# Kernel optimization log

Measured on AMD Instinct MI355X. Metric: run time of the kernel, lower is better.

Reference implementation:

```python
import jax, jax.numpy as jnp
import numpy as np

B, C, H, W = 32, 64, 56, 56
REPN, NK, SMALL = 50, 17, 3   # repN=64-int(64*0.23), nk=ceil(51/3)
GROUPS = 4                     # N_rep
EPS = 1e-5


def _build_index_mats():
    """Reduce the fallback's python scatter-add loops to exact linear maps.
    For flat position p=r*NK+j the roll shifts depend only on p%3, so each
    shift class s gets a (REPN,NK) count matrix over source nk-slots."""
    rng = np.random.RandomState(123)
    ghost = np.sort(rng.choice(C, C - REPN, replace=False))
    rep = np.array(sorted(set(range(C)) - set(ghost.tolist())), np.int32)
    Mh = np.zeros((3, REPN, NK), np.int32)
    Mv = np.zeros((3, REPN, NK), np.int32)
    Mid = np.zeros((REPN, NK), np.int32)
    for _ in range(GROUPS):
        for r in range(REPN):
            perm = rng.permutation(NK)
            for p in range(NK):
                Mh[(r * NK + p) % 3, r, perm[p]] += 1
        for r in range(REPN):
            perm = rng.permutation(NK)
            for p in range(NK):
                Mv[(r * NK + p) % 3, r, perm[p]] += 1
        kk = rng.randint(0, NK, REPN)
        for r in range(REPN):
            Mid[r, kk[r]] += 1
    return ghost.astype(np.int32), rep, Mh, Mv, Mid


def setup_inputs() -> dict:
    key = jax.random.key(0)
    k1, k2, k3 = jax.random.split(key, 3)
    ghost, rep, Mh, Mv, Mid = _build_index_mats()
    return {
        "inputs": jax.random.normal(k1, (B, C, H, W), jnp.float32),
        "w0": jax.random.normal(k2, (REPN * NK, 1, SMALL, SMALL), jnp.float32) * 0.1,
        "w1": jax.random.normal(k3, (REPN * NK, 1, SMALL, SMALL), jnp.float32) * 0.1,
        "Mh": jnp.asarray(Mh), "Mv": jnp.asarray(Mv), "Mid": jnp.asarray(Mid),
        "ghost_idx": jnp.asarray(ghost), "rep_idx": jnp.asarray(rep),
    }


def _bn(x):
    # BatchNorm2d in training mode, affine weight=1 / bias=0 (init values)
    m = x.mean(axis=(0, 2, 3), keepdims=True)
    v = x.var(axis=(0, 2, 3), keepdims=True)
    return (x - m) / jnp.sqrt(v + EPS)


def reference(inputs, w0, w1, Mh, Mv, Mid, ghost_idx, rep_idx):
    rep_in = inputs[:, rep_idx]      # (B, REPN, H, W)
    ghost_in = inputs[:, ghost_idx]  # (B, ghostN, H, W)

    def conv(w):  # depthwise-grouped conv: groups=REPN, each 1->NK channels
        return jax.lax.conv_general_dilated(
            rep_in, w, window_strides=(1, 1), padding=((2, 2), (2, 2)),
            dimension_numbers=('NCHW', 'OIHW', 'NCHW'),
            feature_group_count=REPN)

    out = conv(w0) + conv(w1)                       # (B, REPN*NK, H+2, W+2)
    xv = out.reshape(B, REPN, NK, H + 2, W + 2)

    Mhf, Mvf, Midf = (m.astype(xv.dtype) for m in (Mh, Mv, Mid))
    sh1, sw1 = (0, 1, 2), (0, 2, 1)   # lora1: shifts (i%3, 2i%3)
    sh2, sw2 = (0, 2, 1), (0, 1, 2)   # lora2: shifts (2i%3, i%3)

    lora1 = sum(jnp.roll(jnp.einsum('rk,brkhw->brhw', Mhf[s], xv),
                         (sh1[s], sw1[s]), axis=(2, 3)) for s in range(3))
    lora2 = sum(jnp.roll(jnp.einsum('rk,brkhw->brhw', Mvf[s], xv),
                         (sh2[s], sw2[s]), axis=(2, 3)) for s in range(3))
    small = jnp.einsum('rk,brkhw->brhw', Midf, xv)

    # center-crop back to (H, W): dh = dw = 1
    lora1 = lora1[:, :, 1:1 + H, 1:1 + W]
    lora2 = lora2[:, :, 1:1 + H, 1:1 + W]
    small = small[:, :, 1:1 + H, 1:1 + W]

    x = _bn(lora1) + _bn(lora2) + _bn(small) + rep_in
    return jnp.concatenate([x, ghost_in], axis=1)   # (B, C, H, W)
```

## Files before the change

### kernel.cpp

```cpp
#include <hip/hip_runtime.h>

#define Bn 32
#define Cn 64
#define Hn 56
#define Wn 56
#define REPN 50
#define NKn 17
#define HWn (Hn*Wn)
#define NSTATf 100352.0f
#define EPSf 1e-5f

#define PART_OFF 0
#define WEFF_OFF 9600

#define SEGH 7
#define NTASK 112

__global__ void k_weff(const float* __restrict__ w0, const float* __restrict__ w1,
                       const int* __restrict__ Mh, const int* __restrict__ Mv,
                       const int* __restrict__ Mid, float* __restrict__ ws)
{
    int idx = blockIdx.x * blockDim.x + threadIdx.x;
    if (idx >= REPN*63) return;
    int r   = idx / 63;
    int rem = idx % 63;
    int t   = rem / 9;
    int ij  = rem % 9;
    const int* M = (t < 3) ? (Mh + (t*REPN + r)*NKn)
                 : (t < 6) ? (Mv + ((t-3)*REPN + r)*NKn)
                           : (Mid + r*NKn);
    float acc = 0.f;
    #pragma unroll
    for (int k = 0; k < NKn; ++k)
        acc += (float)M[k] * (w0[(r*NKn + k)*9 + ij] + w1[(r*NKn + k)*9 + ij]);
    ws[WEFF_OFF + idx] = acc;
}

__device__ __forceinline__ void load_row8c(const float* __restrict__ ch, int row, int q,
                                           float* __restrict__ X, float& c55)
{
    bool rv = (row >= 0) && (row < Hn);
    int rc = rv ? row : 0;
    const float* rp = ch + rc*Wn;
    float4 c0 = *(const float4*)(rp + (q ? 4*q - 4 : 0));
    float4 c1 = *(const float4*)(rp + 4*q);
    int ox = (4*q + 4 <= 55) ? 4*q + 4 : 55;
    float cx = rp[ox];
    float mr = rv ? 1.f : 0.f;
    float m0 = (rv && q > 0)  ? 1.f : 0.f;
    float mx = (rv && q < 13) ? 1.f : 0.f;
    X[0]=c0.y*m0; X[1]=c0.z*m0; X[2]=c0.w*m0;
    X[3]=c1.x*mr; X[4]=c1.y*mr; X[5]=c1.z*mr; X[6]=c1.w*mr;
    X[7]=cx*mx;
    c55 = (q == 0) ? rp[55]*mr : 0.f;
}

template <typename F>
__device__ __forceinline__ void conv_walk(const float* __restrict__ ch,
        const float (&wk)[63], int tid, F emit)
{
    if (tid >= NTASK) return;
    int seg = tid / 14;
    int q   = tid - seg*14;
    int h0  = seg * SEGH;
    bool top = (seg == 0);

    float W[5][8], C[5], T[8];
    {
        float dummy;
        if (top) load_row8c(ch, 55, q, T, dummy);
    }
    #pragma unroll
    for (int k = 0; k < 5; ++k)
        load_row8c(ch, h0 - 3 + k, q, W[k], C[k]);

    #pragma unroll
    for (int s = 0; s < SEGH; ++s) {
        int h = h0 + s;
        float Wn8[8], Cn1;
        load_row8c(ch, h + 2, q, Wn8, Cn1);

        float l1[4], l2[4], sm[4];
        #pragma unroll
        for (int p = 0; p < 4; ++p) { l1[p]=0.f; l2[p]=0.f; sm[p]=0.f; }
        #pragma unroll
        for (int i = 0; i < 3; ++i)
            #pragma unroll
            for (int j = 0; j < 3; ++j) {
                float wh0 = wk[i*3+j],    wv0 = wk[27+i*3+j], wid = wk[54+i*3+j];
                float wh1 = wk[9+i*3+j],  wv2 = wk[45+i*3+j];
                float wh2 = wk[18+i*3+j], wv1 = wk[36+i*3+j];
                #pragma unroll
                for (int p = 0; p < 4; ++p) {
                    float a  = W[2+i][p+2+j];
                    l1[p] = fmaf(a, wh0, l1[p]);
                    l2[p] = fmaf(a, wv0, l2[p]);
                    sm[p] = fmaf(a, wid, sm[p]);
                    float bA = W[1+i][p+j];
                    l1[p] = fmaf(bA, wh1, l1[p]);
                    l2[p] = fmaf(bA, wv2, l2[p]);
                    float bB = W[i][p+1+j];
                    l1[p] = fmaf(bB, wh2, l1[p]);
                    l2[p] = fmaf(bB, wv1, l2[p]);
                }
            }
        if (q == 0) {
            #pragma unroll
            for (int i = 0; i < 3; ++i) {
                l1[0] = fmaf(C[1+i], wk[9+3*i],  l1[0]);
                l2[0] = fmaf(C[1+i], wk[45+3*i], l2[0]);
            }
        }
        if (s == 0 && top) {
            #pragma unroll
            for (int j = 0; j < 3; ++j)
                #pragma unroll
                for (int p = 0; p < 4; ++p) {
                    l1[p] = fmaf(T[p+1+j], wk[18+j], l1[p]);
                    l2[p] = fmaf(T[p+1+j], wk[36+j], l2[p]);
                }
        }
        float res[4] = {W[3][3], W[3][4], W[3][5], W[3][6]};
        emit(h, q, l1, l2, sm, res);

        #pragma unroll
        for (int k = 0; k < 4; ++k) {
            #pragma unroll
            for (int x = 0; x < 8; ++x) W[k][x] = W[k+1][x];
            C[k] = C[k+1];
        }
        #pragma unroll
        for (int x = 0; x < 8; ++x) W[4][x] = Wn8[x];
        C[4] = Cn1;
    }
}

__global__ void __launch_bounds__(128) k_stats(const float* __restrict__ in,
        const int* __restrict__ rep_idx, float* __restrict__ ws)
{
    int bid = blockIdx.x;
    int r = bid % REPN;
    int b = bid / REPN;
    int tid = threadIdx.x;

    const float* wr = ws + WEFF_OFF + r*63;
    float wk[63];
    #pragma unroll
    for (int i = 0; i < 63; ++i) wk[i] = wr[i];

    int cin = rep_idx[r];
    const float* ch = in + ((size_t)(b*Cn + cin))*HWn;

    float s1=0.f,q1=0.f,s2=0.f,q2=0.f,s3=0.f,q3=0.f;
    conv_walk(ch, wk, tid,
        [&](int h, int q, float* l1, float* l2, float* sm, float* res) {
            (void)h; (void)q; (void)res;
            #pragma unroll
            for (int p = 0; p < 4; ++p) {
                s1 += l1[p]; q1 += l1[p]*l1[p];
                s2 += l2[p]; q2 += l2[p]*l2[p];
                s3 += sm[p]; q3 += sm[p]*sm[p];
            }
        });

    __shared__ float red[2][6];
    float vals[6] = {s1,q1,s2,q2,s3,q3};
    int lane = tid & 63, wave = tid >> 6;
    #pragma unroll
    for (int v = 0; v < 6; ++v) {
        float x = vals[v];
        for (int o = 32; o; o >>= 1) x += __shfl_down(x, o, 64);
        if (lane == 0) red[wave][v] = x;
    }
    __syncthreads();
    if (tid < 6)
        ws[PART_OFF + (tid*REPN + r)*Bn + b] = red[0][tid] + red[1][tid];
}

__global__ void __launch_bounds__(128) k_out(const float* __restrict__ in,
        const int* __restrict__ rep_idx, const int* __restrict__ ghost_idx,
        const float* __restrict__ ws, float* __restrict__ out)
{
    int bid = blockIdx.x;
    int c = bid % Cn;
    int b = bid / Cn;
    int tid = threadIdx.x;

    if (c >= REPN) {
        int cin = ghost_idx[c - REPN];
        const float4* s4 = (const float4*)(in + ((size_t)(b*Cn + cin))*HWn);
        float4* d4 = (float4*)(out + ((size_t)(b*Cn + c))*HWn);
        for (int i = tid; i < HWn/4; i += 128) d4[i] = s4[i];
        return;
    }

    int r = c;
    __shared__ float sred[6];
    if (tid < 6) {
        const float* pp = ws + PART_OFF + (tid*REPN + r)*Bn;
        float s = 0.f;
        #pragma unroll
        for (int i = 0; i < Bn; ++i) s += pp[i];
        sred[tid] = s;
    }
    __syncthreads();
    const float inv = 1.0f / NSTATf;
    float m1 = sred[0]*inv, v1 = sred[1]*inv - m1*m1;
    float m2 = sred[2]*inv, v2 = sred[3]*inv - m2*m2;
    float m3 = sred[4]*inv, v3 = sred[5]*inv - m3*m3;
    float r1 = rsqrtf(v1 + EPSf), r2 = rsqrtf(v2 + EPSf), r3 = rsqrtf(v3 + EPSf);

    const float* wr = ws + WEFF_OFF + r*63;
    float wk[63];
    #pragma unroll
    for (int i = 0; i < 63; ++i) wk[i] = wr[i];

    int cin = rep_idx[r];
    const float* ch = in + ((size_t)(b*Cn + cin))*HWn;
    float* dst = out + ((size_t)(b*Cn + c))*HWn;

    conv_walk(ch, wk, tid,
        [&](int h, int q, float* l1, float* l2, float* sm, float* res) {
            float4 o;
            o.x = (l1[0]-m1)*r1 + (l2[0]-m2)*r2 + (sm[0]-m3)*r3 + res[0];
            o.y = (l1[1]-m1)*r1 + (l2[1]-m2)*r2 + (sm[1]-m3)*r3 + res[1];
            o.z = (l1[2]-m1)*r1 + (l2[2]-m2)*r2 + (sm[2]-m3)*r3 + res[2];
            o.w = (l1[3]-m1)*r1 + (l2[3]-m2)*r2 + (sm[3]-m3)*r3 + res[3];
            *(float4*)(dst + h*Wn + 4*q) = o;
        });
}

extern "C" void kernel_launch(void* const* d_in, const int* in_sizes, int n_in,
                              void* d_out, int out_size, void* d_ws, size_t ws_size,
                              hipStream_t stream) {
    const float* in   = (const float*)d_in[0];
    const float* w0   = (const float*)d_in[1];
    const float* w1   = (const float*)d_in[2];
    const int*   Mh   = (const int*)d_in[3];
    const int*   Mv   = (const int*)d_in[4];
    const int*   Mid  = (const int*)d_in[5];
    const int*   ghost= (const int*)d_in[6];
    const int*   rep  = (const int*)d_in[7];
    float* out  = (float*)d_out;
    float* ws   = (float*)d_ws;

    k_weff<<<(REPN*63 + 127)/128, 128, 0, stream>>>(w0, w1, Mh, Mv, Mid, ws);
    k_stats<<<Bn*REPN, 128, 0, stream>>>(in, rep, ws);
    k_out<<<Bn*Cn, 128, 0, stream>>>(in, rep, ghost, ws, out);
}
```

Measured before the change: 124.7 us.

## Fuse weight, stats and output kernels into one cooperative persistent kernel

Replaces the three-kernel launch chain with a single cooperative kernel of 1024 blocks that uses grid-wide syncs between the effective-weight, batch-stat and output phases. Each block handles two (batch, channel) slices and falls back to the old launches if occupancy is below four blocks per CU or the cooperative launch fails. The goal is to remove launch gaps and inter-kernel idle time. In exchange, the fixed grid of 1024 blocks with 112 active threads each may limit parallelism, and grid.sync adds its own overhead.

New measurement: 124.3 us. Within noise of the previous version (-0.3%).

```diff
diff --git a/kernel.cpp b/kernel.cpp
--- a/kernel.cpp
+++ b/kernel.cpp
@@ -1,4 +1,7 @@
 #include <hip/hip_runtime.h>
+#include <hip/hip_cooperative_groups.h>
+
+namespace cg = cooperative_groups;
 
 #define Bn 32
 #define Cn 64
@@ -16,12 +19,11 @@
 #define SEGH 7
 #define NTASK 112
 
-__global__ void k_weff(const float* __restrict__ w0, const float* __restrict__ w1,
-                       const int* __restrict__ Mh, const int* __restrict__ Mv,
-                       const int* __restrict__ Mid, float* __restrict__ ws)
-{
-    int idx = blockIdx.x * blockDim.x + threadIdx.x;
-    if (idx >= REPN*63) return;
+__device__ __forceinline__ void weff_one(int idx,
+        const float* __restrict__ w0, const float* __restrict__ w1,
+        const int* __restrict__ Mh, const int* __restrict__ Mv,
+        const int* __restrict__ Mid, float* __restrict__ ws)
+{
     int r   = idx / 63;
     int rem = idx % 63;
     int t   = rem / 9;
@@ -34,6 +36,14 @@
     for (int k = 0; k < NKn; ++k)
         acc += (float)M[k] * (w0[(r*NKn + k)*9 + ij] + w1[(r*NKn + k)*9 + ij]);
     ws[WEFF_OFF + idx] = acc;
+}
+
+__global__ void k_weff(const float* __restrict__ w0, const float* __restrict__ w1,
+                       const int* __restrict__ Mh, const int* __restrict__ Mv,
+                       const int* __restrict__ Mid, float* __restrict__ ws)
+{
+    int idx = blockIdx.x * blockDim.x + threadIdx.x;
+    if (idx < REPN*63) weff_one(idx, w0, w1, Mh, Mv, Mid, ws);
 }
 
 __device__ __forceinline__ void load_row8c(const float* __restrict__ ch, int row, int q,
@@ -135,6 +145,112 @@
     }
 }
 
+__global__ void __launch_bounds__(128, 2) k_fused(const float* __restrict__ in,
+        const float* __restrict__ w0, const float* __restrict__ w1,
+        const int* __restrict__ Mh, const int* __restrict__ Mv,
+        const int* __restrict__ Mid,
+        const int* __restrict__ rep_idx, const int* __restrict__ ghost_idx,
+        float* __restrict__ ws, float* __restrict__ out)
+{
+    cg::grid_group grid = cg::this_grid();
+    int tid = threadIdx.x;
+
+    {
+        int gidx = blockIdx.x * 128 + tid;
+        if (gidx < REPN*63) weff_one(gidx, w0, w1, Mh, Mv, Mid, ws);
+    }
+    grid.sync();
+
+    __shared__ float red[2][6];
+    #pragma unroll
+    for (int it = 0; it < 2; ++it) {
+        int v = blockIdx.x*2 + it;
+        int c = v & 63;
+        int b = v >> 6;
+        if (c >= REPN) {
+            int cin = ghost_idx[c - REPN];
+            const float4* s4 = (const float4*)(in + ((size_t)(b*Cn + cin))*HWn);
+            float4* d4 = (float4*)(out + ((size_t)(b*Cn + c))*HWn);
+            for (int i = tid; i < HWn/4; i += 128) d4[i] = s4[i];
+            continue;
+        }
+        int r = c;
+        const float* wr = ws + WEFF_OFF + r*63;
+        float wk[63];
+        #pragma unroll
+        for (int i = 0; i < 63; ++i) wk[i] = wr[i];
+        const float* ch = in + ((size_t)(b*Cn + rep_idx[r]))*HWn;
+
+        float s1=0.f,q1=0.f,s2=0.f,q2=0.f,s3=0.f,q3=0.f;
+        conv_walk(ch, wk, tid,
+            [&](int h, int q, float* l1, float* l2, float* sm, float* res) {
+                (void)h; (void)q; (void)res;
+                #pragma unroll
+                for (int p = 0; p < 4; ++p) {
+                    s1 += l1[p]; q1 += l1[p]*l1[p];
+                    s2 += l2[p]; q2 += l2[p]*l2[p];
+                    s3 += sm[p]; q3 += sm[p]*sm[p];
+                }
+            });
+        __syncthreads();
+        {
+            float vals[6] = {s1,q1,s2,q2,s3,q3};
+            int lane = tid & 63, wave = tid >> 6;
+            #pragma unroll
+            for (int x = 0; x < 6; ++x) {
+                float y = vals[x];
+                for (int o = 32; o; o >>= 1) y += __shfl_down(y, o, 64);
+                if (lane == 0) red[wave][x] = y;
+            }
+        }
+        __syncthreads();
+        if (tid < 6)
+            ws[PART_OFF + (tid*REPN + r)*Bn + b] = red[0][tid] + red[1][tid];
+    }
+    grid.sync();
+
+    __shared__ float sred[6];
+    #pragma unroll
+    for (int it = 0; it < 2; ++it) {
+        int v = blockIdx.x*2 + it;
+        int c = v & 63;
+        int b = v >> 6;
+        if (c >= REPN) continue;
+        int r = c;
+        __syncthreads();
+        if (tid < 6) {
+            const float* pp = ws + PART_OFF + (tid*REPN + r)*Bn;
+            float s = 0.f;
+            #pragma unroll
+            for (int i = 0; i < Bn; ++i) s += pp[i];
+            sred[tid] = s;
+        }
+        __syncthreads();
+        const float inv = 1.0f / NSTATf;
+        float m1 = sred[0]*inv, v1 = sred[1]*inv - m1*m1;
+        float m2 = sred[2]*inv, v2 = sred[3]*inv - m2*m2;
+        float m3 = sred[4]*inv, v3 = sred[5]*inv - m3*m3;
+        float r1 = rsqrtf(v1 + EPSf), r2 = rsqrtf(v2 + EPSf), r3 = rsqrtf(v3 + EPSf);
+
+        const float* wr = ws + WEFF_OFF + r*63;
+        float wk[63];
+        #pragma unroll
+        for (int i = 0; i < 63; ++i) wk[i] = wr[i];
+        const float* ch = in + ((size_t)(b*Cn + rep_idx[r]))*HWn;
+        float* dst = out + ((size_t)(b*Cn + c))*HWn;
+
+        conv_walk(ch, wk, tid,
+            [&](int h, int q, float* l1, float* l2, float* sm, float* res) {
+                float4 o;
+                o.x = (l1[0]-m1)*r1 + (l2[0]-m2)*r2 + (sm[0]-m3)*r3 + res[0];
+                o.y = (l1[1]-m1)*r1 + (l2[1]-m2)*r2 + (sm[1]-m3)*r3 + res[1];
+                o.z = (l1[2]-m1)*r1 + (l2[2]-m2)*r2 + (sm[2]-m3)*r3 + res[2];
+                o.w = (l1[3]-m1)*r1 + (l2[3]-m2)*r2 + (sm[3]-m3)*r3 + res[3];
+                *(float4*)(dst + h*Wn + 4*q) = o;
+            });
+    }
+}
+
 __global__ void __launch_bounds__(128) k_stats(const float* __restrict__ in,
         const int* __restrict__ rep_idx, float* __restrict__ ws)
 {
@@ -147,9 +263,7 @@
     float wk[63];
     #pragma unroll
     for (int i = 0; i < 63; ++i) wk[i] = wr[i];
-
-    int cin = rep_idx[r];
-    const float* ch = in + ((size_t)(b*Cn + cin))*HWn;
+    const float* ch = in + ((size_t)(b*Cn + rep_idx[r]))*HWn;
 
     float s1=0.f,q1=0.f,s2=0.f,q2=0.f,s3=0.f,q3=0.f;
     conv_walk(ch, wk, tid,
@@ -214,9 +328,7 @@
     float wk[63];
     #pragma unroll
     for (int i = 0; i < 63; ++i) wk[i] = wr[i];
-
-    int cin = rep_idx[r];
-    const float* ch = in + ((size_t)(b*Cn + cin))*HWn;
+    const float* ch = in + ((size_t)(b*Cn + rep_idx[r]))*HWn;
     float* dst = out + ((size_t)(b*Cn + c))*HWn;
 
     conv_walk(ch, wk, tid,
@@ -244,6 +356,19 @@
     float* out  = (float*)d_out;
     float* ws   = (float*)d_ws;
 
+    int maxBlk = 0;
+    hipError_t qerr = hipOccupancyMaxActiveBlocksPerMultiprocessor(
+        &maxBlk, (const void*)k_fused, 128, 0);
+    bool coop_ok = (qerr == hipSuccess) && (maxBlk >= 4);
+
+    if (coop_ok) {
+        void* args[] = { (void*)&in, (void*)&w0, (void*)&w1, (void*)&Mh,
+                         (void*)&Mv, (void*)&Mid, (void*)&rep, (void*)&ghost,
+                         (void*)&ws, (void*)&out };
+        hipError_t lerr = hipLaunchCooperativeKernel((const void*)k_fused,
+                              dim3(1024), dim3(128), args, 0, stream);
+        if (lerr == hipSuccess) return;
+    }
     k_weff<<<(REPN*63 + 127)/128, 128, 0, stream>>>(w0, w1, Mh, Mv, Mid, ws);
     k_stats<<<Bn*REPN, 128, 0, stream>>>(in, rep, ws);
     k_out<<<Bn*Cn, 128, 0, stream>>>(in, rep, ghost, ws, out);
```

## Move ghost-channel copy into stats kernel and process two planes per block

Applied to the files above, without the earlier changes.

The ghost-channel passthrough copy now runs inside the stats kernel, in 224 extra blocks that each copy two planes. The output kernel then handles only the rep channels. Both the stats and output kernels give each block two (batch, channel) planes, which halves the grid sizes and cuts per-block setup cost. This overlaps the copy traffic with the compute-heavy stats pass, but it also adds serial work per block and extra syncthreads.

Result: slower. 139.6 us (+11.9%).

```diff
diff --git a/kernel.cpp b/kernel.cpp
--- a/kernel.cpp
+++ b/kernel.cpp
@@ -136,98 +136,111 @@
 }
 
 __global__ void __launch_bounds__(128) k_stats(const float* __restrict__ in,
-        const int* __restrict__ rep_idx, float* __restrict__ ws)
+        const int* __restrict__ rep_idx, const int* __restrict__ ghost_idx,
+        float* __restrict__ ws, float* __restrict__ out)
 {
     int bid = blockIdx.x;
-    int r = bid % REPN;
-    int b = bid / REPN;
     int tid = threadIdx.x;
 
-    const float* wr = ws + WEFF_OFF + r*63;
-    float wk[63];
-    #pragma unroll
-    for (int i = 0; i < 63; ++i) wk[i] = wr[i];
-
-    int cin = rep_idx[r];
-    const float* ch = in + ((size_t)(b*Cn + cin))*HWn;
-
-    float s1=0.f,q1=0.f,s2=0.f,q2=0.f,s3=0.f,q3=0.f;
-    conv_walk(ch, wk, tid,
-        [&](int h, int q, float* l1, float* l2, float* sm, float* res) {
-            (void)h; (void)q; (void)res;
-            #pragma unroll
-            for (int p = 0; p < 4; ++p) {
-                s1 += l1[p]; q1 += l1[p]*l1[p];
-                s2 += l2[p]; q2 += l2[p]*l2[p];
-                s3 += sm[p]; q3 += sm[p]*sm[p];
+    if (bid >= 800) {
+        for (int it = 0; it < 2; ++it) {
+            int t = (bid - 800)*2 + it;
+            int g = t % 14;
+            int b = t / 14;
+            int cin = ghost_idx[g];
+            const float4* s4 = (const float4*)(in + ((size_t)(b*Cn + cin))*HWn);
+            float4* d4 = (float4*)(out + ((size_t)(b*Cn + REPN + g))*HWn);
+            for (int i = tid; i < HWn/4; i += 128) d4[i] = s4[i];
+        }
+        return;
+    }
+
+    __shared__ float red[2][6];
+    for (int it = 0; it < 2; ++it) {
+        int v = bid*2 + it;
+        int r = v % REPN;
+        int b = v / REPN;
+
+        const float* wr = ws + WEFF_OFF + r*63;
+        float wk[63];
+        #pragma unroll
+        for (int i = 0; i < 63; ++i) wk[i] = wr[i];
+        const float* ch = in + ((size_t)(b*Cn + rep_idx[r]))*HWn;
+
+        float s1=0.f,q1=0.f,s2=0.f,q2=0.f,s3=0.f,q3=0.f;
+        conv_walk(ch, wk, tid,
+            [&](int h, int q, float* l1, float* l2, float* sm, float* res) {
+                (void)h; (void)q; (void)res;
+                #pragma unroll
+                for (int p = 0; p < 4; ++p) {
+                    s1 += l1[p]; q1 += l1[p]*l1[p];
+                    s2 += l2[p]; q2 += l2[p]*l2[p];
+                    s3 += sm[p]; q3 += sm[p]*sm[p];
+                }
+            });
+
+        __syncthreads();
+        {
+            float vals[6] = {s1,q1,s2,q2,s3,q3};
+            int lane = tid & 63, wave = tid >> 6;
+            #pragma unroll
+            for (int x = 0; x < 6; ++x) {
+                float y = vals[x];
+                for (int o = 32; o; o >>= 1) y += __shfl_down(y, o, 64);
+                if (lane == 0) red[wave][x] = y;
             }
-        });
-
-    __shared__ float red[2][6];
-    float vals[6] = {s1,q1,s2,q2,s3,q3};
-    int lane = tid & 63, wave = tid >> 6;
-    #pragma unroll
-    for (int v = 0; v < 6; ++v) {
-        float x = vals[v];
-        for (int o = 32; o; o >>= 1) x += __shfl_down(x, o, 64);
-        if (lane == 0) red[wave][v] = x;
-    }
-    __syncthreads();
-    if (tid < 6)
-        ws[PART_OFF + (tid*REPN + r)*Bn + b] = red[0][tid] + red[1][tid];
+        }
+        __syncthreads();
+        if (tid < 6)
+            ws[PART_OFF + (tid*REPN + r)*Bn + b] = red[0][tid] + red[1][tid];
+    }
 }
 
 __global__ void __launch_bounds__(128) k_out(const float* __restrict__ in,
-        const int* __restrict__ rep_idx, const int* __restrict__ ghost_idx,
-        const float* __restrict__ ws, float* __restrict__ out)
+        const int* __restrict__ rep_idx, const float* __restrict__ ws,
+        float* __restrict__ out)
 {
     int bid = blockIdx.x;
-    int c = bid % Cn;
-    int b = bid / Cn;
     int tid = threadIdx.x;
 
-    if (c >= REPN) {
-        int cin = ghost_idx[c - REPN];
-        const float4* s4 = (const float4*)(in + ((size_t)(b*Cn + cin))*HWn);
-        float4* d4 = (float4*)(out + ((size_t)(b*Cn + c))*HWn);
-        for (int i = tid; i < HWn/4; i += 128) d4[i] = s4[i];
-        return;
-    }
-
-    int r = c;
     __shared__ float sred[6];
-    if (tid < 6) {
-        const float* pp = ws + PART_OFF + (tid*REPN + r)*Bn;
-        float s = 0.f;
-        #pragma unroll
-        for (int i = 0; i < Bn; ++i) s += pp[i];
-        sred[tid] = s;
-    }
-    __syncthreads();
-    const float inv = 1.0f / NSTATf;
-    float m1 = sred[0]*inv, v1 = sred[1]*inv - m1*m1;
-    float m2 = sred[2]*inv, v2 = sred[3]*inv - m2*m2;
-    float m3 = sred[4]*inv, v3 = sred[5]*inv - m3*m3;
-    float r1 = rsqrtf(v1 + EPSf), r2 = rsqrtf(v2 + EPSf), r3 = rsqrtf(v3 + EPSf);
-
-    const float* wr = ws + WEFF_OFF + r*63;
-    float wk[63];
-    #pragma unroll
-    for (int i = 0; i < 63; ++i) wk[i] = wr[i];
-
-    int cin = rep_idx[r];
-    const float* ch = in + ((size_t)(b*Cn + cin))*HWn;
-    float* dst = out + ((size_t)(b*Cn + c))*HWn;
-
-    conv_walk(ch, wk, tid,
-        [&](int h, int q, float* l1, float* l2, float* sm, float* res) {
-            float4 o;
-            o.x = (l1[0]-m1)*r1 + (l2[0]-m2)*r2 + (sm[0]-m3)*r3 + res[0];
-            o.y = (l1[1]-m1)*r1 + (l2[1]-m2)*r2 + (sm[1]-m3)*r3 + res[1];
-            o.z = (l1[2]-m1)*r1 + (l2[2]-m2)*r2 + (sm[2]-m3)*r3 + res[2];
-            o.w = (l1[3]-m1)*r1 + (l2[3]-m2)*r2 + (sm[3]-m3)*r3 + res[3];
-            *(float4*)(dst + h*Wn + 4*q) = o;
-        });
+    for (int it = 0; it < 2; ++it) {
+        int v = bid*2 + it;
+        int r = v % REPN;
+        int b = v / REPN;
+
+        __syncthreads();
+        if (tid < 6) {
+            const float* pp = ws + PART_OFF + (tid*REPN + r)*Bn;
+            float s = 0.f;
+            #pragma unroll
+            for (int i = 0; i < Bn; ++i) s += pp[i];
+            sred[tid] = s;
+        }
+        __syncthreads();
+        const float inv = 1.0f / NSTATf;
+        float m1 = sred[0]*inv, v1 = sred[1]*inv - m1*m1;
+        float m2 = sred[2]*inv, v2 = sred[3]*inv - m2*m2;
+        float m3 = sred[4]*inv, v3 = sred[5]*inv - m3*m3;
+        float r1 = rsqrtf(v1 + EPSf), r2 = rsqrtf(v2 + EPSf), r3 = rsqrtf(v3 + EPSf);
+
+        const float* wr = ws + WEFF_OFF + r*63;
+        float wk[63];
+        #pragma unroll
+        for (int i = 0; i < 63; ++i) wk[i] = wr[i];
+        const float* ch = in + ((size_t)(b*Cn + rep_idx[r]))*HWn;
+        float* dst = out + ((size_t)(b*Cn + r))*HWn;
+
+        conv_walk(ch, wk, tid,
+            [&](int h, int q, float* l1, float* l2, float* sm, float* res) {
+                float4 o;
+                o.x = (l1[0]-m1)*r1 + (l2[0]-m2)*r2 + (sm[0]-m3)*r3 + res[0];
+                o.y = (l1[1]-m1)*r1 + (l2[1]-m2)*r2 + (sm[1]-m3)*r3 + res[1];
+                o.z = (l1[2]-m1)*r1 + (l2[2]-m2)*r2 + (sm[2]-m3)*r3 + res[2];
+                o.w = (l1[3]-m1)*r1 + (l2[3]-m2)*r2 + (sm[3]-m3)*r3 + res[3];
+                *(float4*)(dst + h*Wn + 4*q) = o;
+            });
+    }
 }
 
 extern "C" void kernel_launch(void* const* d_in, const int* in_sizes, int n_in,
@@ -245,6 +258,6 @@
     float* ws   = (float*)d_ws;
 
     k_weff<<<(REPN*63 + 127)/128, 128, 0, stream>>>(w0, w1, Mh, Mv, Mid, ws);
-    k_stats<<<Bn*REPN, 128, 0, stream>>>(in, rep, ws);
-    k_out<<<Bn*Cn, 128, 0, stream>>>(in, rep, ghost, ws, out);
-}
+    k_stats<<<1024, 128, 0, stream>>>(in, rep, ghost, ws, out);
+    k_out<<<800, 128, 0, stream>>>(in, rep, ws, out);
+}
```

## Fuse effective-weight computation into stats kernel and halve segment height

Applied to the files above, without the earlier changes.

Removes the separate weight-folding kernel launch by having each stats block compute its 63 effective weights into shared memory, with the first batch's blocks also writing them to workspace for the output kernel. The row segment per thread drops from 7 to 4 rows, so each channel uses 196 threads in 256-thread blocks instead of 112 in 128-thread blocks, raising parallelism per block. In exchange every stats block redoes the small weight reduction, and shorter segments reload more halo rows per output row.

Result: slower. 129.1 us (+3.5%).

```diff
diff --git a/kernel.cpp b/kernel.cpp
--- a/kernel.cpp
+++ b/kernel.cpp
@@ -13,17 +13,15 @@
 #define PART_OFF 0
 #define WEFF_OFF 9600
 
-#define SEGH 7
-#define NTASK 112
-
-__global__ void k_weff(const float* __restrict__ w0, const float* __restrict__ w1,
-                       const int* __restrict__ Mh, const int* __restrict__ Mv,
-                       const int* __restrict__ Mid, float* __restrict__ ws)
-{
-    int idx = blockIdx.x * blockDim.x + threadIdx.x;
-    if (idx >= REPN*63) return;
-    int r   = idx / 63;
-    int rem = idx % 63;
+#define SEGH 4
+#define NSEG 14
+#define NTASK (NSEG*14)
+
+__device__ __forceinline__ float weff_one(int r, int rem,
+        const float* __restrict__ w0, const float* __restrict__ w1,
+        const int* __restrict__ Mh, const int* __restrict__ Mv,
+        const int* __restrict__ Mid)
+{
     int t   = rem / 9;
     int ij  = rem % 9;
     const int* M = (t < 3) ? (Mh + (t*REPN + r)*NKn)
@@ -33,7 +31,7 @@
     #pragma unroll
     for (int k = 0; k < NKn; ++k)
         acc += (float)M[k] * (w0[(r*NKn + k)*9 + ij] + w1[(r*NKn + k)*9 + ij]);
-    ws[WEFF_OFF + idx] = acc;
+    return acc;
 }
 
 __device__ __forceinline__ void load_row8c(const float* __restrict__ ch, int row, int q,
@@ -135,21 +133,29 @@
     }
 }
 
-__global__ void __launch_bounds__(128) k_stats(const float* __restrict__ in,
-        const int* __restrict__ rep_idx, float* __restrict__ ws)
+__global__ void __launch_bounds__(256) k_stats(const float* __restrict__ in,
+        const float* __restrict__ w0, const float* __restrict__ w1,
+        const int* __restrict__ Mh, const int* __restrict__ Mv,
+        const int* __restrict__ Mid, const int* __restrict__ rep_idx,
+        float* __restrict__ ws)
 {
     int bid = blockIdx.x;
     int r = bid % REPN;
     int b = bid / REPN;
     int tid = threadIdx.x;
 
-    const float* wr = ws + WEFF_OFF + r*63;
+    __shared__ float wkl[63];
+    if (tid < 63) {
+        float v = weff_one(r, tid, w0, w1, Mh, Mv, Mid);
+        wkl[tid] = v;
+        if (bid < REPN) ws[WEFF_OFF + bid*63 + tid] = v;
+    }
+    __syncthreads();
     float wk[63];
     #pragma unroll
-    for (int i = 0; i < 63; ++i) wk[i] = wr[i];
-
-    int cin = rep_idx[r];
-    const float* ch = in + ((size_t)(b*Cn + cin))*HWn;
+    for (int i = 0; i < 63; ++i) wk[i] = wkl[i];
+
+    const float* ch = in + ((size_t)(b*Cn + rep_idx[r]))*HWn;
 
     float s1=0.f,q1=0.f,s2=0.f,q2=0.f,s3=0.f,q3=0.f;
     conv_walk(ch, wk, tid,
@@ -163,21 +169,24 @@
             }
         });
 
-    __shared__ float red[2][6];
-    float vals[6] = {s1,q1,s2,q2,s3,q3};
-    int lane = tid & 63, wave = tid >> 6;
-    #pragma unroll
-    for (int v = 0; v < 6; ++v) {
-        float x = vals[v];
-        for (int o = 32; o; o >>= 1) x += __shfl_down(x, o, 64);
-        if (lane == 0) red[wave][v] = x;
+    __shared__ float red[4][6];
+    {
+        float vals[6] = {s1,q1,s2,q2,s3,q3};
+        int lane = tid & 63, wave = tid >> 6;
+        #pragma unroll
+        for (int v = 0; v < 6; ++v) {
+            float x = vals[v];
+            for (int o = 32; o; o >>= 1) x += __shfl_down(x, o, 64);
+            if (lane == 0) red[wave][v] = x;
+        }
     }
     __syncthreads();
     if (tid < 6)
-        ws[PART_OFF + (tid*REPN + r)*Bn + b] = red[0][tid] + red[1][tid];
-}
-
-__global__ void __launch_bounds__(128) k_out(const float* __restrict__ in,
+        ws[PART_OFF + (tid*REPN + r)*Bn + b] =
+            red[0][tid] + red[1][tid] + red[2][tid] + red[3][tid];
+}
+
+__global__ void __launch_bounds__(256) k_out(const float* __restrict__ in,
         const int* __restrict__ rep_idx, const int* __restrict__ ghost_idx,
         const float* __restrict__ ws, float* __restrict__ out)
 {
@@ -190,7 +199,7 @@
         int cin = ghost_idx[c - REPN];
         const float4* s4 = (const float4*)(in + ((size_t)(b*Cn + cin))*HWn);
         float4* d4 = (float4*)(out + ((size_t)(b*Cn + c))*HWn);
-        for (int i = tid; i < HWn/4; i += 128) d4[i] = s4[i];
+        for (int i = tid; i < HWn/4; i += 256) d4[i] = s4[i];
         return;
     }
 
@@ -215,8 +224,7 @@
     #pragma unroll
     for (int i = 0; i < 63; ++i) wk[i] = wr[i];
 
-    int cin = rep_idx[r];
-    const float* ch = in + ((size_t)(b*Cn + cin))*HWn;
+    const float* ch = in + ((size_t)(b*Cn + rep_idx[r]))*HWn;
     float* dst = out + ((size_t)(b*Cn + c))*HWn;
 
     conv_walk(ch, wk, tid,
@@ -244,7 +252,6 @@
     float* out  = (float*)d_out;
     float* ws   = (float*)d_ws;
 
-    k_weff<<<(REPN*63 + 127)/128, 128, 0, stream>>>(w0, w1, Mh, Mv, Mid, ws);
-    k_stats<<<Bn*REPN, 128, 0, stream>>>(in, rep, ws);
-    k_out<<<Bn*Cn, 128, 0, stream>>>(in, rep, ghost, ws, out);
-}
+    k_stats<<<Bn*REPN, 256, 0, stream>>>(in, w0, w1, Mh, Mv, Mid, rep, ws);
+    k_out<<<Bn*Cn, 256, 0, stream>>>(in, rep, ghost, ws, out);
+}
```
